# Optimization experiments

Hardware: AMD Instinct MI355X
Metric: run time of the kernel (lower is better)

Reference implementation:

```python
import jax, jax.numpy as jnp
import numpy as np

B, L, D = 4, 512, 128

def setup_inputs() -> dict:
    key = jax.random.key(0)
    k1, k2, k3, k4 = jax.random.split(key, 4)
    s = 1.0 / np.sqrt(D)
    return {
        "inp": jax.random.normal(k1, (B, L, D), dtype=jnp.float32),
        "Wu": jax.random.normal(k2, (D, D), dtype=jnp.float32) * s,
        "Ww": jax.random.normal(k3, (D, D), dtype=jnp.float32) * s,
        "Wv": jax.random.normal(k4, (1, D), dtype=jnp.float32) * s,
    }

def reference(inp, Wu, Ww, Wv):
    # inp: (B,L,D); torch Linear weights are (out,in), so y = x @ W.T
    qu = inp @ Wu.T                      # (B,L,D), u(inp)
    kw = inp @ Ww.T                      # (B,L,D), w(inp)
    # qu.unsqueeze(1) -> broadcast over i; kw.unsqueeze(2) -> broadcast over j
    # h[b,i,j,:] = tanh(u(inp)[b,j] + w(inp)[b,i])   (dropout = identity in eval)
    h = jnp.tanh(qu[:, None, :, :] + kw[:, :, None, :])   # (B,L,L,D)
    score = jnp.einsum('bijd,d->bij', h, Wv[0])           # (B,L,L)
    attn = jax.nn.softmax(score, axis=2)                  # softmax over keys j
    out = jnp.einsum('bij,bjd->bid', attn, inp)           # bmm(attn, inp)
    return out, attn
```

## Files before the change

kernel.cpp:

```cpp
#include <hip/hip_runtime.h>

#define BD 128
#define SL 512
#define NB 4

__device__ __forceinline__ float rcp_fast(float x) { return __builtin_amdgcn_rcpf(x); }

__global__ __launch_bounds__(256) void k_tr(const float* __restrict__ Wu,
                                            const float* __restrict__ Ww,
                                            float* __restrict__ WuT,
                                            float* __restrict__ WwT) {
    int idx = blockIdx.x * 256 + threadIdx.x;
    int k = idx >> 7, o = idx & 127;
    WuT[idx] = Wu[o * BD + k];
    WwT[idx] = Ww[o * BD + k];
}

__global__ __launch_bounds__(256) void k_qk(const float* __restrict__ inp,
                                            const float* __restrict__ WuT,
                                            const float* __restrict__ WwT,
                                            float* __restrict__ Equ,
                                            float* __restrict__ Ekw) {
    __shared__ float sx[4][BD];
    const int t = threadIdx.x, m = t >> 7, o = t & 127;
    const int r0 = blockIdx.x * 4;
    const int b  = r0 >> 9;
    const int l0 = r0 & (SL - 1);

    #pragma unroll
    for (int h = 0; h < 2; ++h) {
        int id = h * 256 + t;
        sx[id >> 7][id & 127] = inp[(size_t)r0 * BD + id];
    }
    __syncthreads();

    const float* WT = m ? WwT : WuT;
    float acc[4] = {0.f, 0.f, 0.f, 0.f};
    #pragma unroll 2
    for (int k = 0; k < BD; k += 4) {
        float w0 = WT[(k + 0) * BD + o];
        float w1 = WT[(k + 1) * BD + o];
        float w2 = WT[(k + 2) * BD + o];
        float w3 = WT[(k + 3) * BD + o];
        #pragma unroll
        for (int rr = 0; rr < 4; ++rr) {
            float4 x = *(const float4*)&sx[rr][k];
            acc[rr] = fmaf(x.x, w0, acc[rr]);
            acc[rr] = fmaf(x.y, w1, acc[rr]);
            acc[rr] = fmaf(x.z, w2, acc[rr]);
            acc[rr] = fmaf(x.w, w3, acc[rr]);
        }
    }

    if (m == 0) {
        #pragma unroll
        for (int rr = 0; rr < 4; ++rr)
            Equ[(((size_t)b * 32 + (o >> 2)) * SL + (l0 + rr)) * 4 + (o & 3)] =
                __expf(2.f * acc[rr]);
    } else {
        #pragma unroll
        for (int rr = 0; rr < 4; ++rr)
            Ekw[(size_t)(r0 + rr) * BD + o] = __expf(2.f * acc[rr]);
    }
}

__global__ __launch_bounds__(1024, 8) void k_attn(const float* __restrict__ inp,
                                                  const float* __restrict__ Wv,
                                                  const float* __restrict__ Equ,
                                                  const float* __restrict__ Ekw,
                                                  float* __restrict__ out,
                                                  float* __restrict__ attn) {
    __shared__ float4 smem4[(SL * 4 + 16 * 4 * BD) / 4];
    float* smem  = (float*)smem4;
    float* s_pT  = smem;
    float* ovl   = smem + SL * 4;
    float4* s_e  = (float4*)ovl;
    float*  s_wv = ovl + 512;
    float*  s_ap = ovl + 640;
    float*  s_red= ovl + 640 + 4 * SL;
    float*  s_fin= ovl;

    const int t  = threadIdx.x;
    const int b  = blockIdx.x >> 7;
    const int i0 = (blockIdx.x & 127) * 4;

    if (t < BD) {
        const float* ek = Ekw + ((size_t)b * SL + i0) * BD + t;
        s_e[t]  = make_float4(ek[0], ek[BD], ek[2 * BD], ek[3 * BD]);
        s_wv[t] = Wv[t];
    }
    __syncthreads();

    const int j = t & 511, dh = t >> 9;
    const float4* equ4 = (const float4*)(Equ + (size_t)b * BD * SL);
    float a[4] = {0.f, 0.f, 0.f, 0.f};
    #pragma unroll 4
    for (int cc = 0; cc < 16; ++cc) {
        int c = dh * 16 + cc;
        float4 q = equ4[c * SL + j];
        float qs[4] = {q.x, q.y, q.z, q.w};
        #pragma unroll
        for (int dd = 0; dd < 4; ++dd) {
            int d = c * 4 + dd;
            float4 e = s_e[d];
            float  w = s_wv[d];
            float  qd = qs[dd];
            a[0] = fmaf(w, rcp_fast(fmaf(qd, e.x, 1.f)), a[0]);
            a[1] = fmaf(w, rcp_fast(fmaf(qd, e.y, 1.f)), a[1]);
            a[2] = fmaf(w, rcp_fast(fmaf(qd, e.z, 1.f)), a[2]);
            a[3] = fmaf(w, rcp_fast(fmaf(qd, e.w, 1.f)), a[3]);
        }
    }

    const int ro = dh * 2, wo = 2 - ro;
    s_ap[(wo + 0) * SL + j] = a[wo + 0];
    s_ap[(wo + 1) * SL + j] = a[wo + 1];
    __syncthreads();
    float af[2] = { a[ro + 0] + s_ap[(ro + 0) * SL + j],
                    a[ro + 1] + s_ap[(ro + 1) * SL + j] };

    const int w8 = j >> 6;
    float mn[2] = { af[0], af[1] };
    #pragma unroll
    for (int off = 32; off > 0; off >>= 1) {
        mn[0] = fminf(mn[0], __shfl_xor(mn[0], off, 64));
        mn[1] = fminf(mn[1], __shfl_xor(mn[1], off, 64));
    }
    if ((j & 63) == 0) { s_red[(ro + 0) * 8 + w8] = mn[0]; s_red[(ro + 1) * 8 + w8] = mn[1]; }
    __syncthreads();
    #pragma unroll
    for (int ii = 0; ii < 2; ++ii) {
        float4 r0 = *(const float4*)&s_red[(ro + ii) * 8];
        float4 r1 = *(const float4*)&s_red[(ro + ii) * 8 + 4];
        mn[ii] = fminf(fminf(fminf(r0.x, r0.y), fminf(r0.z, r0.w)),
                       fminf(fminf(r1.x, r1.y), fminf(r1.z, r1.w)));
    }

    float p[2] = { __expf(-2.f * (af[0] - mn[0])), __expf(-2.f * (af[1] - mn[1])) };
    float sm[2] = { p[0], p[1] };
    #pragma unroll
    for (int off = 32; off > 0; off >>= 1) {
        sm[0] += __shfl_xor(sm[0], off, 64);
        sm[1] += __shfl_xor(sm[1], off, 64);
    }
    __syncthreads();
    if ((j & 63) == 0) { s_red[(ro + 0) * 8 + w8] = sm[0]; s_red[(ro + 1) * 8 + w8] = sm[1]; }
    __syncthreads();
    float n[2];
    #pragma unroll
    for (int ii = 0; ii < 2; ++ii) {
        float4 r0 = *(const float4*)&s_red[(ro + ii) * 8];
        float4 r1 = *(const float4*)&s_red[(ro + ii) * 8 + 4];
        float rs = rcp_fast((r0.x + r0.y) + (r0.z + r0.w) + (r1.x + r1.y) + (r1.z + r1.w));
        n[ii] = p[ii] * rs;
        attn[((size_t)b * SL + i0 + ro + ii) * SL + j] = n[ii];
    }
    ((float2*)s_pT)[j * 2 + dh] = make_float2(n[0], n[1]);
    __syncthreads();

    const int g  = t >> 6;
    const int ln = t & 63;
    const int dq = ln & 31;
    const int rh = ln >> 5;
    const float4* inp4 = (const float4*)(inp + (size_t)b * SL * BD);
    float4 acc0 = make_float4(0.f, 0.f, 0.f, 0.f);
    float4 acc1 = make_float4(0.f, 0.f, 0.f, 0.f);
    #pragma unroll 4
    for (int jj = 0; jj < 32; ++jj) {
        int jr = g * 32 + jj;
        float4 x  = inp4[jr * 32 + dq];
        float2 pp = ((const float2*)s_pT)[jr * 2 + rh];
        acc0.x = fmaf(pp.x, x.x, acc0.x); acc0.y = fmaf(pp.x, x.y, acc0.y);
        acc0.z = fmaf(pp.x, x.z, acc0.z); acc0.w = fmaf(pp.x, x.w, acc0.w);
        acc1.x = fmaf(pp.y, x.x, acc1.x); acc1.y = fmaf(pp.y, x.y, acc1.y);
        acc1.z = fmaf(pp.y, x.z, acc1.z); acc1.w = fmaf(pp.y, x.w, acc1.w);
    }
    *(float4*)&s_fin[((g * 4) + rh * 2 + 0) * BD + dq * 4] = acc0;
    *(float4*)&s_fin[((g * 4) + rh * 2 + 1) * BD + dq * 4] = acc1;
    __syncthreads();
    if (t < 512) {
        int row = t >> 7, d = t & 127;
        float s = 0.f;
        #pragma unroll
        for (int gg = 0; gg < 16; ++gg)
            s += s_fin[(gg * 4 + row) * BD + d];
        out[((size_t)b * SL + i0 + row) * BD + d] = s;
    }
}

extern "C" void kernel_launch(void* const* d_in, const int* in_sizes, int n_in,
                              void* d_out, int out_size, void* d_ws, size_t ws_size,
                              hipStream_t stream) {
    const float* inp = (const float*)d_in[0];
    const float* Wu  = (const float*)d_in[1];
    const float* Ww  = (const float*)d_in[2];
    const float* Wv  = (const float*)d_in[3];

    float* out  = (float*)d_out;
    float* attn = out + (size_t)NB * SL * BD;

    float* ws  = (float*)d_ws;
    float* Equ = ws;
    float* Ekw = Equ + (size_t)NB * BD * SL;
    float* WuT = Ekw + (size_t)NB * SL * BD;
    float* WwT = WuT + BD * BD;

    k_tr  <<<BD * BD / 256, 256, 0, stream>>>(Wu, Ww, WuT, WwT);
    k_qk  <<<NB * SL / 4, 256, 0, stream>>>(inp, WuT, WwT, Equ, Ekw);
    k_attn<<<NB * SL / 4, 1024, 0, stream>>>(inp, Wv, Equ, Ekw, out, attn);
}
```

Measured before the change: 95.83 us.

## Fold Wv into exp-kw factors and restructure attention score accumulation

Rewrites each tanh score term as 1/(q*E/w + 1/w), so the Wv weight is folded into precomputed shared factors and the inner loop becomes fma+rcp+add. Equ is stored interleaved by key pairs so each thread processes two keys over a quarter of the feature dimension, with a four-way shared-memory reduction afterwards. k_qk now uses two rows per block, doubling its block count, and separate reduction buffers remove one barrier. Dividing by Wv can lose precision or hit infinities when weights are near zero.

```diff
diff --git a/kernel.cpp b/kernel.cpp
--- a/kernel.cpp
+++ b/kernel.cpp
@@ -19,119 +19,133 @@
 __global__ __launch_bounds__(256) void k_qk(const float* __restrict__ inp,
                                             const float* __restrict__ WuT,
                                             const float* __restrict__ WwT,
-                                            float* __restrict__ Equ,
+                                            float* __restrict__ Equ2,
                                             float* __restrict__ Ekw) {
-    __shared__ float sx[4][BD];
+    __shared__ float sx[2][BD];
     const int t = threadIdx.x, m = t >> 7, o = t & 127;
-    const int r0 = blockIdx.x * 4;
+    const int r0 = blockIdx.x * 2;
     const int b  = r0 >> 9;
     const int l0 = r0 & (SL - 1);
-
-    #pragma unroll
-    for (int h = 0; h < 2; ++h) {
-        int id = h * 256 + t;
-        sx[id >> 7][id & 127] = inp[(size_t)r0 * BD + id];
-    }
+    const int jp = l0 >> 1;
+
+    sx[t >> 7][t & 127] = inp[(size_t)r0 * BD + t];
     __syncthreads();
 
     const float* WT = m ? WwT : WuT;
-    float acc[4] = {0.f, 0.f, 0.f, 0.f};
-    #pragma unroll 2
+    float acc0 = 0.f, acc1 = 0.f;
+    #pragma unroll 4
     for (int k = 0; k < BD; k += 4) {
         float w0 = WT[(k + 0) * BD + o];
         float w1 = WT[(k + 1) * BD + o];
         float w2 = WT[(k + 2) * BD + o];
         float w3 = WT[(k + 3) * BD + o];
-        #pragma unroll
-        for (int rr = 0; rr < 4; ++rr) {
-            float4 x = *(const float4*)&sx[rr][k];
-            acc[rr] = fmaf(x.x, w0, acc[rr]);
-            acc[rr] = fmaf(x.y, w1, acc[rr]);
-            acc[rr] = fmaf(x.z, w2, acc[rr]);
-            acc[rr] = fmaf(x.w, w3, acc[rr]);
-        }
+        float4 x0 = *(const float4*)&sx[0][k];
+        float4 x1 = *(const float4*)&sx[1][k];
+        acc0 = fmaf(x0.x, w0, acc0); acc0 = fmaf(x0.y, w1, acc0);
+        acc0 = fmaf(x0.z, w2, acc0); acc0 = fmaf(x0.w, w3, acc0);
+        acc1 = fmaf(x1.x, w0, acc1); acc1 = fmaf(x1.y, w1, acc1);
+        acc1 = fmaf(x1.z, w2, acc1); acc1 = fmaf(x1.w, w3, acc1);
     }
 
     if (m == 0) {
-        #pragma unroll
-        for (int rr = 0; rr < 4; ++rr)
-            Equ[(((size_t)b * 32 + (o >> 2)) * SL + (l0 + rr)) * 4 + (o & 3)] =
-                __expf(2.f * acc[rr]);
+        size_t base = (((size_t)b * 32 + (o >> 2)) * 256 + jp) * 8 + (o & 3);
+        Equ2[base]     = __expf(2.f * acc0);
+        Equ2[base + 4] = __expf(2.f * acc1);
     } else {
-        #pragma unroll
-        for (int rr = 0; rr < 4; ++rr)
-            Ekw[(size_t)(r0 + rr) * BD + o] = __expf(2.f * acc[rr]);
+        Ekw[(size_t)(r0 + 0) * BD + o] = __expf(2.f * acc0);
+        Ekw[(size_t)(r0 + 1) * BD + o] = __expf(2.f * acc1);
     }
 }
 
 __global__ __launch_bounds__(1024, 8) void k_attn(const float* __restrict__ inp,
                                                   const float* __restrict__ Wv,
-                                                  const float* __restrict__ Equ,
+                                                  const float* __restrict__ Equ2,
                                                   const float* __restrict__ Ekw,
                                                   float* __restrict__ out,
                                                   float* __restrict__ attn) {
-    __shared__ float4 smem4[(SL * 4 + 16 * 4 * BD) / 4];
+    __shared__ float4 smem4[(SL * 4 + 8960) / 4];
     float* smem  = (float*)smem4;
     float* s_pT  = smem;
     float* ovl   = smem + SL * 4;
-    float4* s_e  = (float4*)ovl;
-    float*  s_wv = ovl + 512;
-    float*  s_ap = ovl + 640;
-    float*  s_red= ovl + 640 + 4 * SL;
+    float4* s_E  = (float4*)ovl;
+    float*  s_u  = ovl + 512;
+    float*  s_ap = ovl;
+    float*  s_rA = ovl + 8704;
+    float*  s_rB = ovl + 8736;
     float*  s_fin= ovl;
 
     const int t  = threadIdx.x;
     const int b  = blockIdx.x >> 7;
     const int i0 = (blockIdx.x & 127) * 4;
 
+    float4 eE; float eu;
     if (t < BD) {
         const float* ek = Ekw + ((size_t)b * SL + i0) * BD + t;
-        s_e[t]  = make_float4(ek[0], ek[BD], ek[2 * BD], ek[3 * BD]);
-        s_wv[t] = Wv[t];
-    }
-    __syncthreads();
-
-    const int j = t & 511, dh = t >> 9;
-    const float4* equ4 = (const float4*)(Equ + (size_t)b * BD * SL);
-    float a[4] = {0.f, 0.f, 0.f, 0.f};
-    #pragma unroll 4
-    for (int cc = 0; cc < 16; ++cc) {
-        int c = dh * 16 + cc;
-        float4 q = equ4[c * SL + j];
-        float qs[4] = {q.x, q.y, q.z, q.w};
+        float e0 = ek[0], e1 = ek[BD], e2 = ek[2 * BD], e3 = ek[3 * BD];
+        eu = rcp_fast(Wv[t]);
+        eE = make_float4(e0 * eu, e1 * eu, e2 * eu, e3 * eu);
+    }
+    if (t < BD) { s_E[t] = eE; s_u[t] = eu; }
+    __syncthreads();
+
+    const int jp = t & 255, dg = t >> 8;
+    const float4* equ4 = (const float4*)(Equ2 + (size_t)b * BD * SL);
+    float a0[4] = {0.f, 0.f, 0.f, 0.f};
+    float a1[4] = {0.f, 0.f, 0.f, 0.f};
+    #pragma unroll 2
+    for (int cc = 0; cc < 8; ++cc) {
+        int c = dg * 8 + cc;
+        float4 qA = equ4[(c * 256 + jp) * 2 + 0];
+        float4 qB = equ4[(c * 256 + jp) * 2 + 1];
+        float qa[4] = {qA.x, qA.y, qA.z, qA.w};
+        float qb[4] = {qB.x, qB.y, qB.z, qB.w};
         #pragma unroll
         for (int dd = 0; dd < 4; ++dd) {
             int d = c * 4 + dd;
-            float4 e = s_e[d];
-            float  w = s_wv[d];
-            float  qd = qs[dd];
-            a[0] = fmaf(w, rcp_fast(fmaf(qd, e.x, 1.f)), a[0]);
-            a[1] = fmaf(w, rcp_fast(fmaf(qd, e.y, 1.f)), a[1]);
-            a[2] = fmaf(w, rcp_fast(fmaf(qd, e.z, 1.f)), a[2]);
-            a[3] = fmaf(w, rcp_fast(fmaf(qd, e.w, 1.f)), a[3]);
+            float4 E = s_E[d];
+            float  u = s_u[d];
+            a0[0] += rcp_fast(fmaf(qa[dd], E.x, u));
+            a0[1] += rcp_fast(fmaf(qa[dd], E.y, u));
+            a0[2] += rcp_fast(fmaf(qa[dd], E.z, u));
+            a0[3] += rcp_fast(fmaf(qa[dd], E.w, u));
+            a1[0] += rcp_fast(fmaf(qb[dd], E.x, u));
+            a1[1] += rcp_fast(fmaf(qb[dd], E.y, u));
+            a1[2] += rcp_fast(fmaf(qb[dd], E.z, u));
+            a1[3] += rcp_fast(fmaf(qb[dd], E.w, u));
         }
     }
-
-    const int ro = dh * 2, wo = 2 - ro;
-    s_ap[(wo + 0) * SL + j] = a[wo + 0];
-    s_ap[(wo + 1) * SL + j] = a[wo + 1];
-    __syncthreads();
-    float af[2] = { a[ro + 0] + s_ap[(ro + 0) * SL + j],
-                    a[ro + 1] + s_ap[(ro + 1) * SL + j] };
-
-    const int w8 = j >> 6;
+    __syncthreads();
+    #pragma unroll
+    for (int i = 0; i < 4; ++i) {
+        s_ap[((dg * 2 + 0) * 4 + i) * 256 + jp] = a0[i];
+        s_ap[((dg * 2 + 1) * 4 + i) * 256 + jp] = a1[i];
+    }
+    __syncthreads();
+
+    const int j = t & 511, dh = t >> 9, ro = dh * 2;
+    const int jpp = j >> 1, jj = j & 1, w8 = j >> 6;
+    float af[2];
+    #pragma unroll
+    for (int ii = 0; ii < 2; ++ii) {
+        int r = ro + ii;
+        af[ii] = s_ap[((0 * 2 + jj) * 4 + r) * 256 + jpp]
+               + s_ap[((1 * 2 + jj) * 4 + r) * 256 + jpp]
+               + s_ap[((2 * 2 + jj) * 4 + r) * 256 + jpp]
+               + s_ap[((3 * 2 + jj) * 4 + r) * 256 + jpp];
+    }
+
     float mn[2] = { af[0], af[1] };
     #pragma unroll
     for (int off = 32; off > 0; off >>= 1) {
         mn[0] = fminf(mn[0], __shfl_xor(mn[0], off, 64));
         mn[1] = fminf(mn[1], __shfl_xor(mn[1], off, 64));
     }
-    if ((j & 63) == 0) { s_red[(ro + 0) * 8 + w8] = mn[0]; s_red[(ro + 1) * 8 + w8] = mn[1]; }
+    if ((j & 63) == 0) { s_rA[(ro + 0) * 8 + w8] = mn[0]; s_rA[(ro + 1) * 8 + w8] = mn[1]; }
     __syncthreads();
     #pragma unroll
     for (int ii = 0; ii < 2; ++ii) {
-        float4 r0 = *(const float4*)&s_red[(ro + ii) * 8];
-        float4 r1 = *(const float4*)&s_red[(ro + ii) * 8 + 4];
+        float4 r0 = *(const float4*)&s_rA[(ro + ii) * 8];
+        float4 r1 = *(const float4*)&s_rA[(ro + ii) * 8 + 4];
         mn[ii] = fminf(fminf(fminf(r0.x, r0.y), fminf(r0.z, r0.w)),
                        fminf(fminf(r1.x, r1.y), fminf(r1.z, r1.w)));
     }
@@ -143,14 +157,13 @@
         sm[0] += __shfl_xor(sm[0], off, 64);
         sm[1] += __shfl_xor(sm[1], off, 64);
     }
-    __syncthreads();
-    if ((j & 63) == 0) { s_red[(ro + 0) * 8 + w8] = sm[0]; s_red[(ro + 1) * 8 + w8] = sm[1]; }
+    if ((j & 63) == 0) { s_rB[(ro + 0) * 8 + w8] = sm[0]; s_rB[(ro + 1) * 8 + w8] = sm[1]; }
     __syncthreads();
     float n[2];
     #pragma unroll
     for (int ii = 0; ii < 2; ++ii) {
-        float4 r0 = *(const float4*)&s_red[(ro + ii) * 8];
-        float4 r1 = *(const float4*)&s_red[(ro + ii) * 8 + 4];
+        float4 r0 = *(const float4*)&s_rB[(ro + ii) * 8];
+        float4 r1 = *(const float4*)&s_rB[(ro + ii) * 8 + 4];
         float rs = rcp_fast((r0.x + r0.y) + (r0.z + r0.w) + (r1.x + r1.y) + (r1.z + r1.w));
         n[ii] = p[ii] * rs;
         attn[((size_t)b * SL + i0 + ro + ii) * SL + j] = n[ii];
@@ -166,8 +179,8 @@
     float4 acc0 = make_float4(0.f, 0.f, 0.f, 0.f);
     float4 acc1 = make_float4(0.f, 0.f, 0.f, 0.f);
     #pragma unroll 4
-    for (int jj = 0; jj < 32; ++jj) {
-        int jr = g * 32 + jj;
+    for (int jjj = 0; jjj < 32; ++jjj) {
+        int jr = g * 32 + jjj;
         float4 x  = inp4[jr * 32 + dq];
         float2 pp = ((const float2*)s_pT)[jr * 2 + rh];
         acc0.x = fmaf(pp.x, x.x, acc0.x); acc0.y = fmaf(pp.x, x.y, acc0.y);
@@ -199,13 +212,13 @@
     float* out  = (float*)d_out;
     float* attn = out + (size_t)NB * SL * BD;
 
-    float* ws  = (float*)d_ws;
-    float* Equ = ws;
-    float* Ekw = Equ + (size_t)NB * BD * SL;
-    float* WuT = Ekw + (size_t)NB * SL * BD;
-    float* WwT = WuT + BD * BD;
+    float* ws   = (float*)d_ws;
+    float* Equ2 = ws;
+    float* Ekw  = Equ2 + (size_t)NB * BD * SL;
+    float* WuT  = Ekw + (size_t)NB * SL * BD;
+    float* WwT  = WuT + BD * BD;
 
     k_tr  <<<BD * BD / 256, 256, 0, stream>>>(Wu, Ww, WuT, WwT);
-    k_qk  <<<NB * SL / 4, 256, 0, stream>>>(inp, WuT, WwT, Equ, Ekw);
-    k_attn<<<NB * SL / 4, 1024, 0, stream>>>(inp, Wv, Equ, Ekw, out, attn);
-}
+    k_qk  <<<NB * SL / 2, 256, 0, stream>>>(inp, WuT, WwT, Equ2, Ekw);
+    k_attn<<<NB * SL / 4, 1024, 0, stream>>>(inp, Wv, Equ2, Ekw, out, attn);
+}
```

Result: no change. 94.94 us (-0.9%).
